# Optimization experiments

Hardware: AMD Instinct MI355X
Metric: run time of the kernel (lower is better)

## Reference

```python
import jax, jax.numpy as jnp
import numpy as np

EPS = 1e-5

def avg_pool3s2(x):
    # AvgPool2d(kernel=3, stride=2, no padding) on NCHW
    s = jax.lax.reduce_window(x, 0.0, jax.lax.add, (1, 1, 3, 3), (1, 1, 2, 2), 'VALID')
    return s / 9.0

def conv1x1(x, W):
    # x: [n,c,h,w], W: [out,c]
    return jnp.einsum('nchw,oc->nohw', x, W)

def batchnorm(x, g, b):
    # training-mode BN over (N,H,W), biased variance (matches torch normalization)
    m = x.mean(axis=(0, 2, 3), keepdims=True)
    v = x.var(axis=(0, 2, 3), keepdims=True)
    return (x - m) * jax.lax.rsqrt(v + EPS) * g[None, :, None, None] + b[None, :, None, None]

def coord_features(hp, wp):
    # [8, hp, wp]: xmin, ymin, xmax, ymax, xctr, yctr, 1/W, 1/H
    w = jnp.arange(wp, dtype=jnp.float32)
    h = jnp.arange(hp, dtype=jnp.float32)
    xmin = w / wp * 2 - 1
    xmax = (w + 1) / wp * 2 - 1
    xctr = (xmin + xmax) / 2
    ymin = h / hp * 2 - 1
    ymax = (h + 1) / hp * 2 - 1
    yctr = (ymin + ymax) / 2
    bx = lambda a: jnp.broadcast_to(a[None, :], (hp, wp))
    by = lambda a: jnp.broadcast_to(a[:, None], (hp, wp))
    const = lambda v: jnp.full((hp, wp), v, dtype=jnp.float32)
    return jnp.stack([bx(xmin), by(ymin), bx(xmax), by(ymax), bx(xctr), by(yctr),
                      const(1.0 / wp), const(1.0 / hp)], axis=0)

def resize_bilinear_ac(x, H, W):
    # bilinear upsample with align_corners=True, x: [n,c,h,w]
    h, w = x.shape[2], x.shape[3]
    ys = jnp.linspace(0.0, h - 1.0, H)
    xs = jnp.linspace(0.0, w - 1.0, W)
    y0 = jnp.floor(ys).astype(jnp.int32); y1 = jnp.minimum(y0 + 1, h - 1); wy = (ys - y0)[None, None, :, None]
    x0 = jnp.floor(xs).astype(jnp.int32); x1 = jnp.minimum(x0 + 1, w - 1); wx = (xs - x0)[None, None, None, :]
    rows = x[:, :, y0, :] * (1 - wy) + x[:, :, y1, :] * wy          # [n,c,H,w]
    return rows[:, :, :, x0] * (1 - wx) + rows[:, :, :, x1] * wx    # [n,c,H,W]

def setup_inputs() -> dict:
    key = jax.random.key(0)
    ks = jax.random.split(key, 8)
    n, in_dim, hid, h, w = 4, 256, 10, 129, 129
    d = hid + 8  # 18
    return {
        'p_fea': jax.random.normal(ks[0], (n, in_dim, h, w), dtype=jnp.float32),
        'hu': jax.random.normal(ks[1], (n, hid, h, w), dtype=jnp.float32),
        'Wq': jax.random.normal(ks[2], (d, d), dtype=jnp.float32) * 0.05,
        'Wk': jax.random.normal(ks[3], (d, in_dim + 8), dtype=jnp.float32) * 0.05,
        'Wv': jax.random.normal(ks[4], (128, in_dim), dtype=jnp.float32) * 0.05,
        'g_v': jnp.ones((128,), dtype=jnp.float32),
        'b_v': jnp.zeros((128,), dtype=jnp.float32),
        'Wp': jax.random.normal(ks[5], (hid, 128), dtype=jnp.float32) * 0.05,
        'g_p': jnp.ones((hid,), dtype=jnp.float32),
        'b_p': jnp.zeros((hid,), dtype=jnp.float32),
    }

def reference(p_fea, hu, Wq, Wk, Wv, g_v, b_v, Wp, g_p, b_p):
    n, c, h, w = p_fea.shape
    p = avg_pool3s2(p_fea)   # [n,256,hp,wp]
    u = avg_pool3s2(hu)      # [n,10,hp,wp]
    hp, wp = p.shape[2], p.shape[3]
    L = hp * wp
    coord = jnp.broadcast_to(coord_features(hp, wp)[None], (n, 8, hp, wp))
    query = conv1x1(jnp.concatenate([u, coord], axis=1), Wq).reshape(n, -1, L).transpose(0, 2, 1)  # [n,L,18]
    key_t = conv1x1(jnp.concatenate([p, coord], axis=1), Wk).reshape(n, -1, L)                      # [n,18,L]
    val = jax.nn.relu(batchnorm(conv1x1(p, Wv), g_v, b_v)).reshape(n, 128, L)                       # [n,128,L]
    energy = jnp.einsum('nlc,ncm->nlm', query, key_t)            # [n,L,L]
    attn = jax.nn.softmax(energy, axis=-1)
    ctx = jnp.einsum('ncm,nlm->ncl', val, attn).reshape(n, 128, hp, wp)
    ctx = jax.nn.relu(batchnorm(conv1x1(ctx, Wp), g_p, b_p))     # [n,10,hp,wp]
    return resize_bilinear_ac(ctx, h, w)                          # [n,10,h,w]
```

## Files before the change

kernel.cpp:

```cpp
#include <hip/hip_runtime.h>
#include <hip/hip_bf16.h>
#include <cstdint>

#define NN   4
#define LL   4096
#define DD   18
#define CVV  128
#define CIN  256
#define CUU  10
#define HH   129
#define COO  10

typedef unsigned short ushort_t;
typedef __attribute__((ext_vector_type(8))) short short8v;
typedef __attribute__((ext_vector_type(4))) short short4v;
typedef __attribute__((ext_vector_type(4))) float f32x4;

#define PB_OFF   ((size_t)0)
#define OP_OFF   ((size_t)2097152)
#define VAL_OFF  ((size_t)2260992)
#define QT_OFF   ((size_t)3309568)
#define KT_OFF   ((size_t)3571712)
#define VT_OFF   ((size_t)3833856)
#define VSC_OFF  ((size_t)4882432)
#define VSH_OFF  ((size_t)4882560)
#define S2_OFF   ((size_t)4882688)
#define SH2_OFF  ((size_t)4882704)
#define PART_OFF ((size_t)4882720)
#define PART2_OFF ((size_t)4915488)
#define KMAX_OFF ((size_t)4916768)

static __device__ __forceinline__ ushort_t f2bf(float x) {
    unsigned int u = __float_as_uint(x);
    unsigned int r = (u + 0x7fffu + ((u >> 16) & 1u)) >> 16;
    return (ushort_t)r;
}
static __device__ __forceinline__ float bf2f(ushort_t b) {
    return __uint_as_float(((unsigned int)b) << 16);
}
static __device__ __forceinline__ unsigned int pk2(float a, float b) {
    return (unsigned int)f2bf(a) | ((unsigned int)f2bf(b) << 16);
}

static __device__ __forceinline__ void gload16(const void* g, void* l) {
    __builtin_amdgcn_global_load_lds(
        (const __attribute__((address_space(1))) void*)g,
        (__attribute__((address_space(3))) void*)l, 16, 0, 0);
}

__global__ __launch_bounds__(256) void pool_bf_kernel(const float* __restrict__ src,
                                                      ushort_t* __restrict__ dst,
                                                      int* __restrict__ kz) {
    if (kz != nullptr && blockIdx.x == 0 && threadIdx.x < 128) kz[threadIdx.x] = 0;
    int b = blockIdx.x;
    int plane = b >> 4;
    int rg = b & 15;
    __shared__ float rows[9][132];
    const float* sp = src + (size_t)plane * (HH * HH) + (size_t)(rg * 8) * HH;
    #pragma unroll
    for (int j = 0; j < 9; ++j) {
        if (threadIdx.x < HH) rows[j][threadIdx.x] = sp[(size_t)j * HH + threadIdx.x];
    }
    __syncthreads();
    int row = threadIdx.x >> 6, ow = threadIdx.x & 63;
    const float* r0 = rows[2 * row];
    const float* r1 = rows[2 * row + 1];
    const float* r2 = rows[2 * row + 2];
    int x = 2 * ow;
    float sum = r0[x] + r0[x + 1] + r0[x + 2]
              + r1[x] + r1[x + 1] + r1[x + 2]
              + r2[x] + r2[x + 1] + r2[x + 2];
    dst[(size_t)plane * 4096 + (size_t)(rg * 4 + row) * 64 + ow] = f2bf(sum * (1.0f / 9.0f));
}

__global__ __launch_bounds__(256, 2) void qkval_kernel(const ushort_t* __restrict__ pb,
                                                       const float* __restrict__ hu,
                                                       const float* __restrict__ Wq,
                                                       const float* __restrict__ Wk,
                                                       const float* __restrict__ Wv,
                                                       ushort_t* __restrict__ qt,
                                                       char* __restrict__ kt_c,
                                                       int* __restrict__ kmaxb,
                                                       ushort_t* __restrict__ val,
                                                       float* __restrict__ part) {
    __shared__ __align__(16) char smem[36864];
    int tid = threadIdx.x;

    if (blockIdx.x < 256) {
        float (*kacc)[64][21] = (float(*)[64][21])smem;
        int n = blockIdx.x >> 6;
        int mb = blockIdx.x & 63;
        int mloc = tid & 63;
        int cs = tid >> 6;
        int m = mb * 64 + mloc;
        int hi = m >> 6, wi = m & 63;

        float coord[8];
        coord[0] = wi * (2.0f / 64.0f) - 1.0f;
        coord[1] = hi * (2.0f / 64.0f) - 1.0f;
        coord[2] = (wi + 1) * (2.0f / 64.0f) - 1.0f;
        coord[3] = (hi + 1) * (2.0f / 64.0f) - 1.0f;
        coord[4] = 0.5f * (coord[0] + coord[2]);
        coord[5] = 0.5f * (coord[1] + coord[3]);
        coord[6] = 1.0f / 64.0f;
        coord[7] = 1.0f / 64.0f;

        {
            float acc[DD];
            #pragma unroll
            for (int o = 0; o < DD; ++o) acc[o] = 0.0f;
            const ushort_t* pc = pb + ((size_t)(n * CIN + cs * 64)) * LL + m;
            for (int c0 = 0; c0 < 64; ++c0) {
                float pv = bf2f(pc[(size_t)c0 * LL]);
                const float* wr = Wk + (cs * 64 + c0);
                #pragma unroll
                for (int o = 0; o < DD; ++o) acc[o] = fmaf(pv, wr[o * 264], acc[o]);
            }
            if (cs == 3) {
                #pragma unroll
                for (int j = 0; j < 8; ++j) {
                    float cv = coord[j];
                    #pragma unroll
                    for (int o = 0; o < DD; ++o) acc[o] = fmaf(cv, Wk[o * 264 + CIN + j], acc[o]);
                }
            }
            #pragma unroll
            for (int o = 0; o < DD; ++o) kacc[cs][mloc][o] = acc[o];
        }
        if (cs == 0) {
            float acc[DD];
            #pragma unroll
            for (int o = 0; o < DD; ++o) acc[o] = 0.0f;
            const float* hub = hu + ((size_t)(n * CUU)) * (HH * HH) + (size_t)(2 * hi) * HH + 2 * wi;
            for (int cq = 0; cq < CUU; ++cq) {
                const float* s = hub + (size_t)cq * (HH * HH);
                float uv = (s[0] + s[1] + s[2]
                          + s[HH] + s[HH + 1] + s[HH + 2]
                          + s[2 * HH] + s[2 * HH + 1] + s[2 * HH + 2]) * (1.0f / 9.0f);
                #pragma unroll
                for (int o = 0; o < DD; ++o) acc[o] = fmaf(uv, Wq[o * DD + cq], acc[o]);
            }
            #pragma unroll
            for (int j = 0; j < 8; ++j) {
                float cv = coord[j];
                #pragma unroll
                for (int o = 0; o < DD; ++o) acc[o] = fmaf(cv, Wq[o * DD + CUU + j], acc[o]);
            }
            union { short8v v[4]; ushort_t s[32]; } pk;
            #pragma unroll
            for (int o = 0; o < 32; ++o) pk.s[o] = (o < DD) ? f2bf(acc[o]) : (ushort_t)0;
            short8v* qrow = (short8v*)(qt + ((size_t)(n * LL) + m) * 32);
            #pragma unroll
            for (int j = 0; j < 4; ++j) qrow[j] = pk.v[j];
        }
        __syncthreads();
        {
            int j = cs;
            union { short8v v; ushort_t s[8]; } pk;
            #pragma unroll
            for (int i = 0; i < 8; ++i) {
                int o = j * 8 + i;
                float v = 0.0f;
                if (o < DD)
                    v = kacc[0][mloc][o] + kacc[1][mloc][o] + kacc[2][mloc][o] + kacc[3][mloc][o];
                pk.s[i] = (o < DD) ? f2bf(v) : (ushort_t)0;
            }
            int byte = ((mloc << 6) | (j << 4)) ^ (((mloc >> 1) & 7) << 4);
            *(short8v*)(kt_c + (size_t)n * 262144 + (size_t)mb * 4096 + byte) = pk.v;

            int mb8[8];
            #pragma unroll
            for (int i = 0; i < 8; ++i) mb8[i] = (int)(pk.s[i] & 0x7fffu);
            #pragma unroll
            for (int off = 1; off < 64; off <<= 1) {
                #pragma unroll
                for (int i = 0; i < 8; ++i) {
                    int ov = __shfl_xor(mb8[i], off);
                    mb8[i] = max(mb8[i], ov);
                }
            }
            if (mloc == 0) {
                #pragma unroll
                for (int i = 0; i < 8; ++i)
                    atomicMax(&kmaxb[n * 32 + cs * 8 + i], mb8[i] << 16);
            }
        }
    } else {
        float (*Wt)[36] = (float(*)[36])smem;
        int b = blockIdx.x - 256;
        int n  = b >> 7;
        int cb = (b >> 5) & 3;
        int mb = b & 31;
        int cg = tid >> 5;
        int mg = tid & 31;
        int ch0 = cb * 32;
        int m0 = mb * 128;

        {
            int c4 = tid & 63;
            int chq = tid >> 6;
            #pragma unroll
            for (int j = 0; j < 8; ++j) {
                int ch = chq * 8 + j;
                float4 v = *(const float4*)&Wv[(size_t)(ch0 + ch) * CIN + c4 * 4];
                Wt[c4 * 4 + 0][ch] = v.x;
                Wt[c4 * 4 + 1][ch] = v.y;
                Wt[c4 * 4 + 2][ch] = v.z;
                Wt[c4 * 4 + 3][ch] = v.w;
            }
        }
        __syncthreads();

        const ushort_t* pbb = pb + (size_t)n * CIN * LL + m0 + mg * 4;
        f32x4 a0 = {0.f,0.f,0.f,0.f}, a1 = {0.f,0.f,0.f,0.f};
        f32x4 a2 = {0.f,0.f,0.f,0.f}, a3 = {0.f,0.f,0.f,0.f};

        #pragma unroll 4
        for (int c = 0; c < CIN; ++c) {
            short4v ps = *(const short4v*)(pbb + (size_t)c * LL);
            f32x4 pv;
            pv[0] = bf2f((ushort_t)ps[0]); pv[1] = bf2f((ushort_t)ps[1]);
            pv[2] = bf2f((ushort_t)ps[2]); pv[3] = bf2f((ushort_t)ps[3]);
            f32x4 wv = *(const f32x4*)&Wt[c][cg * 4];
            a0 += pv * wv.x;
            a1 += pv * wv.y;
            a2 += pv * wv.z;
            a3 += pv * wv.w;
        }

        size_t out = ((size_t)(n * CVV + ch0 + cg * 4)) * LL + m0 + mg * 4;
        union { short4v v; ushort_t s[4]; } w0, w1, w2, w3;
        #pragma unroll
        for (int i = 0; i < 4; ++i) {
            w0.s[i] = f2bf(a0[i]); w1.s[i] = f2bf(a1[i]);
            w2.s[i] = f2bf(a2[i]); w3.s[i] = f2bf(a3[i]);
        }
        *(short4v*)&val[out]          = w0.v;
        *(short4v*)&val[out + LL]     = w1.v;
        *(short4v*)&val[out + 2*LL]   = w2.v;
        *(short4v*)&val[out + 3*LL]   = w3.v;

        float s1[4], s2[4];
        s1[0] = a0[0]+a0[1]+a0[2]+a0[3]; s2[0] = a0[0]*a0[0]+a0[1]*a0[1]+a0[2]*a0[2]+a0[3]*a0[3];
        s1[1] = a1[0]+a1[1]+a1[2]+a1[3]; s2[1] = a1[0]*a1[0]+a1[1]*a1[1]+a1[2]*a1[2]+a1[3]*a1[3];
        s1[2] = a2[0]+a2[1]+a2[2]+a2[3]; s2[2] = a2[0]*a2[0]+a2[1]*a2[1]+a2[2]*a2[2]+a2[3]*a2[3];
        s1[3] = a3[0]+a3[1]+a3[2]+a3[3]; s2[3] = a3[0]*a3[0]+a3[1]*a3[1]+a3[2]*a3[2]+a3[3]*a3[3];
        #pragma unroll
        for (int off = 1; off < 32; off <<= 1) {
            #pragma unroll
            for (int i = 0; i < 4; ++i) {
                s1[i] += __shfl_xor(s1[i], off);
                s2[i] += __shfl_xor(s2[i], off);
            }
        }
        if (mg == 0) {
            #pragma unroll
            for (int i = 0; i < 4; ++i) {
                part[(((size_t)b * 8 + cg) * 4 + i) * 2]     = s1[i];
                part[(((size_t)b * 8 + cg) * 4 + i) * 2 + 1] = s2[i];
            }
        }
    }
}

__global__ __launch_bounds__(128) void bn_finalize_v_kernel(const float* __restrict__ part,
                                                            const float* __restrict__ g,
                                                            const float* __restrict__ bta,
                                                            float* __restrict__ scale,
                                                            float* __restrict__ shift) {
    int ch = threadIdx.x;
    if (ch >= CVV) return;
    int cb = ch >> 5;
    int cg = (ch & 31) >> 2;
    int i = ch & 3;
    float s1 = 0.0f, s2 = 0.0f;
    for (int n = 0; n < NN; ++n) {
        for (int mb = 0; mb < 32; ++mb) {
            int b = n * 128 + cb * 32 + mb;
            size_t idx = (((size_t)b * 8 + cg) * 4 + i) * 2;
            s1 += part[idx];
            s2 += part[idx + 1];
        }
    }
    float mean = s1 * (1.0f / (NN * LL));
    float var = s2 * (1.0f / (NN * LL)) - mean * mean;
    float inv = rsqrtf(var + 1e-5f);
    float sc = g[ch] * inv;
    scale[ch] = sc;
    shift[ch] = bta[ch] - mean * sc;
}

__global__ __launch_bounds__(256) void bn_apply2_kernel(const ushort_t* __restrict__ val,
                                                        const float* __restrict__ scale,
                                                        const float* __restrict__ shift,
                                                        char* __restrict__ vt_c) {
    int t = blockIdx.x * 256 + threadIdx.x;
    int mq = t & 511;
    int ch = (t >> 9) & 127;
    int n = t >> 16;
    int m0 = mq * 8;
    short8v vs = *(const short8v*)(val + ((size_t)(n * CVV + ch)) * LL + m0);
    float sc = scale[ch], sh = shift[ch];
    union { short8v v; ushort_t s[8]; } pk;
    #pragma unroll
    for (int i = 0; i < 8; ++i)
        pk.s[i] = f2bf(fmaxf(fmaf(bf2f((ushort_t)vs[i]), sc, sh), 0.0f));
    int tile = m0 >> 5, mloc = m0 & 31;
    size_t byte = (size_t)n * 1048576 + (size_t)tile * 8192
                + (size_t)(((ch << 6) | (mloc << 1)) ^ ((ch & 7) << 4));
    *(short8v*)(vt_c + byte) = pk.v;
}

__global__ __launch_bounds__(256, 4) void attn_swz_kernel(const ushort_t* __restrict__ qt,
                                                          const char* __restrict__ kt_c,
                                                          const char* __restrict__ vt_c,
                                                          const int* __restrict__ kmaxb,
                                                          const float* __restrict__ Wp,
                                                          float* __restrict__ ypart,
                                                          float* __restrict__ Lp) {
    int orig = blockIdx.x;
    int xcd = orig & 7;
    int idx = orig >> 3;
    int qb = idx >> 1;
    int combo = xcd * 2 + (idx & 1);
    int n = combo >> 2;
    int sM = combo & 3;
    int T0 = sM * 32;

    int tid = threadIdx.x;
    int w = tid >> 6, lane = tid & 63, c = lane & 15, g = lane >> 4;
    int l0w = qb * 64 + w * 16;

    __shared__ __align__(16) ushort_t K_t[2][1024];
    __shared__ __align__(16) ushort_t V_t[2][4096];
    __shared__ __align__(16) uint4 exch[4][64];
    __shared__ float Wpl[COO][CVV];

    for (int i = tid; i < COO * CVV; i += 256) Wpl[i >> 7][i & 127] = Wp[i];

    const char* ktb = kt_c + (size_t)n * 262144;
    const char* vtb = vt_c + (size_t)n * 1048576;

    short8v qf = *(const short8v*)(qt + (((size_t)n * LL + l0w + c) << 5) + g * 8);
    int vxor = (c & 7) << 4;

    float Mq = 0.0f;
    {
        const int* km = kmaxb + n * 32 + g * 8;
        #pragma unroll
        for (int i = 0; i < 8; ++i) {
            float kv = __int_as_float(km[i]);
            float aq = __uint_as_float(((unsigned int)((ushort_t)qf[i]) & 0x7fffu) << 16);
            Mq = fmaf(aq, kv, Mq);
        }
        Mq += __shfl_xor(Mq, 16);
        Mq += __shfl_xor(Mq, 32);
    }

    f32x4 O[8];
    #pragma unroll
    for (int i = 0; i < 8; ++i) O[i] = (f32x4){0.f, 0.f, 0.f, 0.f};
    float Lacc = 0.0f;

    int kby0, kby1;
    {
        int kr0 = c, kr1 = 16 + c;
        kby0 = ((kr0 << 6) | (g << 4)) ^ (((kr0 >> 1) & 7) << 4);
        kby1 = ((kr1 << 6) | (g << 4)) ^ (((kr1 >> 1) & 7) << 4);
    }
    int srcA = ((g & 1) << 5) + c;
    int toff = (g >> 1) * 8;

    {
        int T = T0;
        const char* ks = ktb + (size_t)(T >> 1) * 4096 + (T & 1) * 2048 + w * 1024 + lane * 16;
        if (w < 2) gload16(ks, (char*)K_t[0] + w * 1024);
        const char* vs = vtb + (size_t)T * 8192 + w * 2048 + lane * 16;
        gload16(vs, (char*)V_t[0] + w * 2048);
        gload16(vs + 1024, (char*)V_t[0] + w * 2048 + 1024);
    }
    __syncthreads();
    int buf = 0;
    for (int mt = 0; mt < 32; ++mt) {
        if (mt + 1 < 32) {
            int T = T0 + mt + 1;
            const char* ks = ktb + (size_t)(T >> 1) * 4096 + (T & 1) * 2048 + w * 1024 + lane * 16;
            if (w < 2) gload16(ks, (char*)K_t[buf ^ 1] + w * 1024);
            const char* vs = vtb + (size_t)T * 8192 + w * 2048 + lane * 16;
            gload16(vs, (char*)V_t[buf ^ 1] + w * 2048);
            gload16(vs + 1024, (char*)V_t[buf ^ 1] + w * 2048 + 1024);
        }
        const char* kb = (const char*)K_t[buf];
        short8v kf0 = *(const short8v*)(kb + kby0);
        short8v kf1 = *(const short8v*)(kb + kby1);
        f32x4 S0 = __builtin_amdgcn_mfma_f32_16x16x32_bf16(kf0, qf, (f32x4){0.f,0.f,0.f,0.f}, 0, 0, 0);
        f32x4 S1 = __builtin_amdgcn_mfma_f32_16x16x32_bf16(kf1, qf, (f32x4){0.f,0.f,0.f,0.f}, 0, 0, 0);
        float p0[4], p1[4];
        #pragma unroll
        for (int r = 0; r < 4; ++r) {
            p0[r] = __expf(S0[r] - Mq);
            p1[r] = __expf(S1[r] - Mq);
            Lacc += p0[r] + p1[r];
        }
        exch[w][lane] = (uint4){ pk2(p0[0], p0[1]), pk2(p0[2], p0[3]),
                                 pk2(p1[0], p1[1]), pk2(p1[2], p1[3]) };
        const char* eb = (const char*)&exch[w][0];
        uint2 ua = *(const uint2*)(eb + srcA * 16 + toff);
        uint2 ub = *(const uint2*)(eb + (srcA + 16) * 16 + toff);
        union { unsigned int u[4]; short8v v; } pa;
        pa.u[0] = ua.x; pa.u[1] = ua.y; pa.u[2] = ub.x; pa.u[3] = ub.y;
        const char* vb = (const char*)V_t[buf];
        __builtin_amdgcn_s_setprio(1);
        #pragma unroll
        for (int ct = 0; ct < 8; ++ct) {
            int vby = (((ct * 16 + c) << 6) | (g << 4)) ^ vxor;
            short8v vf = *(const short8v*)(vb + vby);
            O[ct] = __builtin_amdgcn_mfma_f32_16x16x32_bf16(pa.v, vf, O[ct], 0, 0, 0);
        }
        __builtin_amdgcn_s_setprio(0);
        __syncthreads();
        buf ^= 1;
    }
    Lacc += __shfl_xor(Lacc, 16);
    Lacc += __shfl_xor(Lacc, 32);
    if (g == 0)
        Lp[sM * (NN * LL) + n * LL + l0w + c] = Lacc;

    float yp[COO][4];
    #pragma unroll
    for (int o = 0; o < COO; ++o)
        #pragma unroll
        for (int r = 0; r < 4; ++r) yp[o][r] = 0.0f;
    #pragma unroll
    for (int ct = 0; ct < 8; ++ct) {
        #pragma unroll
        for (int o = 0; o < COO; ++o) {
            float wv = Wpl[o][ct * 16 + c];
            #pragma unroll
            for (int r = 0; r < 4; ++r)
                yp[o][r] = fmaf(O[ct][r], wv, yp[o][r]);
        }
    }
    #pragma unroll
    for (int off = 1; off < 16; off <<= 1) {
        #pragma unroll
        for (int o = 0; o < COO; ++o)
            #pragma unroll
            for (int r = 0; r < 4; ++r)
                yp[o][r] += __shfl_xor(yp[o][r], off);
    }
    if (c == 0) {
        #pragma unroll
        for (int r = 0; r < 4; ++r) {
            size_t yrow = (size_t)(sM * (NN * LL) + n * LL + l0w + g * 4 + r);
            #pragma unroll
            for (int o = 0; o < COO; ++o)
                ypart[yrow * COO + o] = yp[o][r];
        }
    }
}

__global__ __launch_bounds__(256) void combine4b_kernel(const float* __restrict__ ypart,
                                                        const float* __restrict__ Lp,
                                                        float* __restrict__ out_pre,
                                                        float* __restrict__ part2) {
    int idx = blockIdx.x * 256 + threadIdx.x;
    int n = idx >> 12;
    int l = idx & 4095;
    int nl = n * LL + l;
    float inv = 1.0f / (Lp[nl] + Lp[16384 + nl] + Lp[2 * 16384 + nl] + Lp[3 * 16384 + nl]);
    const float* y0 = ypart + (size_t)nl * COO;
    const float* y1 = ypart + ((size_t)16384 + nl) * COO;
    const float* y2 = ypart + ((size_t)(2 * 16384) + nl) * COO;
    const float* y3 = ypart + ((size_t)(3 * 16384) + nl) * COO;
    float ov[COO];
    #pragma unroll
    for (int o = 0; o < COO; ++o) {
        ov[o] = (y0[o] + y1[o] + y2[o] + y3[o]) * inv;
        out_pre[((size_t)(n * COO + o)) * LL + l] = ov[o];
    }
    float p1[COO], p2[COO];
    #pragma unroll
    for (int o = 0; o < COO; ++o) { p1[o] = ov[o]; p2[o] = ov[o] * ov[o]; }
    #pragma unroll
    for (int off = 1; off < 64; off <<= 1) {
        #pragma unroll
        for (int o = 0; o < COO; ++o) {
            p1[o] += __shfl_xor(p1[o], off);
            p2[o] += __shfl_xor(p2[o], off);
        }
    }
    __shared__ float rs1[4][COO], rs2[4][COO];
    int w = threadIdx.x >> 6, lane = threadIdx.x & 63;
    if (lane == 0) {
        #pragma unroll
        for (int o = 0; o < COO; ++o) { rs1[w][o] = p1[o]; rs2[w][o] = p2[o]; }
    }
    __syncthreads();
    if (threadIdx.x < COO) {
        int o = threadIdx.x;
        float a = rs1[0][o] + rs1[1][o] + rs1[2][o] + rs1[3][o];
        float b = rs2[0][o] + rs2[1][o] + rs2[2][o] + rs2[3][o];
        part2[((size_t)blockIdx.x * COO + o) * 2]     = a;
        part2[((size_t)blockIdx.x * COO + o) * 2 + 1] = b;
    }
}

__global__ __launch_bounds__(64) void bn_finalize2_kernel(const float* __restrict__ part2,
                                                          const float* __restrict__ g,
                                                          const float* __restrict__ bta,
                                                          float* __restrict__ scale,
                                                          float* __restrict__ shift) {
    int ch = threadIdx.x;
    if (ch >= COO) return;
    float s1 = 0.0f, s2 = 0.0f;
    for (int b = 0; b < 64; ++b) {
        s1 += part2[((size_t)b * COO + ch) * 2];
        s2 += part2[((size_t)b * COO + ch) * 2 + 1];
    }
    float mean = s1 * (1.0f / (NN * LL));
    float var = s2 * (1.0f / (NN * LL)) - mean * mean;
    float inv = rsqrtf(var + 1e-5f);
    float sc = g[ch] * inv;
    scale[ch] = sc;
    shift[ch] = bta[ch] - mean * sc;
}

__global__ __launch_bounds__(256) void resize_kernel(const float* __restrict__ out_pre,
                                                     const float* __restrict__ scale,
                                                     const float* __restrict__ shift,
                                                     float* __restrict__ out,
                                                     int total) {
    int idx = blockIdx.x * 256 + threadIdx.x;
    if (idx >= total) return;
    int ow = idx % HH;
    int t = idx / HH;
    int oh = t % HH;
    int t2 = t / HH;
    int o = t2 % COO;
    int n = t2 / COO;

    const float r = 63.0f / 128.0f;
    float y = oh * r;
    float x = ow * r;
    int y0 = (int)y;
    int x0 = (int)x;
    float wy = y - y0;
    float wx = x - x0;
    int y1 = min(y0 + 1, 63);
    int x1 = min(x0 + 1, 63);

    const float* base = out_pre + ((size_t)(n * COO + o)) * LL;
    float sc = scale[o], sh = shift[o];
    float v00 = fmaxf(fmaf(base[y0 * 64 + x0], sc, sh), 0.0f);
    float v01 = fmaxf(fmaf(base[y0 * 64 + x1], sc, sh), 0.0f);
    float v10 = fmaxf(fmaf(base[y1 * 64 + x0], sc, sh), 0.0f);
    float v11 = fmaxf(fmaf(base[y1 * 64 + x1], sc, sh), 0.0f);
    float top = v00 * (1.0f - wx) + v01 * wx;
    float bot = v10 * (1.0f - wx) + v11 * wx;
    out[idx] = top * (1.0f - wy) + bot * wy;
}

extern "C" void kernel_launch(void* const* d_in, const int* in_sizes, int n_in,
                              void* d_out, int out_size, void* d_ws, size_t ws_size,
                              hipStream_t stream) {
    (void)in_sizes; (void)n_in; (void)out_size; (void)ws_size;
    const float* p_fea = (const float*)d_in[0];
    const float* hu    = (const float*)d_in[1];
    const float* Wq    = (const float*)d_in[2];
    const float* Wk    = (const float*)d_in[3];
    const float* Wv    = (const float*)d_in[4];
    const float* g_v   = (const float*)d_in[5];
    const float* b_v   = (const float*)d_in[6];
    const float* Wp    = (const float*)d_in[7];
    const float* g_p   = (const float*)d_in[8];
    const float* b_p   = (const float*)d_in[9];

    float* ws = (float*)d_ws;
    ushort_t* pbb     = (ushort_t*)(ws + PB_OFF);
    float*    out_pre = ws + OP_OFF;
    ushort_t* valb    = (ushort_t*)(ws + VAL_OFF);
    ushort_t* qtb     = (ushort_t*)(ws + QT_OFF);
    char*     ktb     = (char*)(ws + KT_OFF);
    char*     vtb     = (char*)(ws + VT_OFF);
    float*    Lpart   = ws + VAL_OFF;
    float*    ypart   = ws + VAL_OFF + 65536;
    float*    vscale  = ws + VSC_OFF;
    float*    vshift  = ws + VSH_OFF;
    float*    scale2  = ws + S2_OFF;
    float*    shift2  = ws + SH2_OFF;
    float*    part    = ws + PART_OFF;
    float*    part2   = ws + PART2_OFF;
    int*      kmaxb   = (int*)(ws + KMAX_OFF);

    pool_bf_kernel<<<NN * CIN * 16, 256, 0, stream>>>(p_fea, pbb, kmaxb);
    qkval_kernel<<<768, 256, 0, stream>>>(pbb, hu, Wq, Wk, Wv, qtb, ktb, kmaxb, valb, part);
    bn_finalize_v_kernel<<<1, 128, 0, stream>>>(part, g_v, b_v, vscale, vshift);
    bn_apply2_kernel<<<(NN * CVV * 512) / 256, 256, 0, stream>>>(valb, vscale, vshift, vtb);
    attn_swz_kernel<<<1024, 256, 0, stream>>>(qtb, ktb, vtb, kmaxb, Wp, ypart, Lpart);
    combine4b_kernel<<<(NN * LL) / 256, 256, 0, stream>>>(ypart, Lpart, out_pre, part2);
    bn_finalize2_kernel<<<1, 64, 0, stream>>>(part2, g_p, b_p, scale2, shift2);
    {
        int total = NN * COO * HH * HH;
        resize_kernel<<<(total + 255) / 256, 256, 0, stream>>>(out_pre, scale2, shift2,
                                                               (float*)d_out, total);
    }
}
```

Measured before the change: 140.5 us.

## Pool into channel-interleaved layout and compute value conv with bf16 MFMA

The pooling kernel now handles 8 channels per block and writes the pooled features in a channel-interleaved [n, c/8, L, 8] bf16 layout with 16-byte stores. The value 1x1 conv drops its scalar FMA loop in favor of 16x16x32 bf16 MFMA instructions that read this layout directly, and the K projection reads 8 channels per vector load. BN partial sums are reorganized per block and channel, and the finalize kernel is updated to match. Weights are rounded to bf16 on the fly, which adds some rounding error, and the value output is now written as scattered 2-byte stores.

```diff
diff --git a/kernel.cpp b/kernel.cpp
--- a/kernel.cpp
+++ b/kernel.cpp
@@ -13,10 +13,9 @@
 
 typedef unsigned short ushort_t;
 typedef __attribute__((ext_vector_type(8))) short short8v;
-typedef __attribute__((ext_vector_type(4))) short short4v;
 typedef __attribute__((ext_vector_type(4))) float f32x4;
 
-#define PB_OFF   ((size_t)0)
+#define PT_OFF   ((size_t)0)
 #define OP_OFF   ((size_t)2097152)
 #define VAL_OFF  ((size_t)2260992)
 #define QT_OFF   ((size_t)3309568)
@@ -27,8 +26,8 @@
 #define S2_OFF   ((size_t)4882688)
 #define SH2_OFF  ((size_t)4882704)
 #define PART_OFF ((size_t)4882720)
-#define PART2_OFF ((size_t)4915488)
-#define KMAX_OFF ((size_t)4916768)
+#define PART2_OFF ((size_t)4948256)
+#define KMAX_OFF ((size_t)4949536)
 
 static __device__ __forceinline__ ushort_t f2bf(float x) {
     unsigned int u = __float_as_uint(x);
@@ -48,42 +47,54 @@
         (__attribute__((address_space(3))) void*)l, 16, 0, 0);
 }
 
-__global__ __launch_bounds__(256) void pool_bf_kernel(const float* __restrict__ src,
-                                                      ushort_t* __restrict__ dst,
+__global__ __launch_bounds__(256) void pool_pt_kernel(const float* __restrict__ src,
+                                                      ushort_t* __restrict__ pt,
                                                       int* __restrict__ kz) {
     if (kz != nullptr && blockIdx.x == 0 && threadIdx.x < 128) kz[threadIdx.x] = 0;
     int b = blockIdx.x;
-    int plane = b >> 4;
     int rg = b & 15;
-    __shared__ float rows[9][132];
-    const float* sp = src + (size_t)plane * (HH * HH) + (size_t)(rg * 8) * HH;
-    #pragma unroll
-    for (int j = 0; j < 9; ++j) {
-        if (threadIdx.x < HH) rows[j][threadIdx.x] = sp[(size_t)j * HH + threadIdx.x];
+    int cg = (b >> 4) & 31;
+    int n  = b >> 9;
+
+    __shared__ float rows[8][9][132];
+    const float* base = src + ((size_t)(n * CIN + cg * 8)) * (HH * HH) + (size_t)(rg * 8) * HH;
+    for (int t = threadIdx.x; t < 8 * 9 * 132; t += 256) {
+        int col = t % 132;
+        int rr  = (t / 132) % 9;
+        int ch  = t / (132 * 9);
+        if (col < HH)
+            rows[ch][rr][col] = base[(size_t)ch * (HH * HH) + (size_t)rr * HH + col];
     }
     __syncthreads();
+
     int row = threadIdx.x >> 6, ow = threadIdx.x & 63;
-    const float* r0 = rows[2 * row];
-    const float* r1 = rows[2 * row + 1];
-    const float* r2 = rows[2 * row + 2];
     int x = 2 * ow;
-    float sum = r0[x] + r0[x + 1] + r0[x + 2]
-              + r1[x] + r1[x + 1] + r1[x + 2]
-              + r2[x] + r2[x + 1] + r2[x + 2];
-    dst[(size_t)plane * 4096 + (size_t)(rg * 4 + row) * 64 + ow] = f2bf(sum * (1.0f / 9.0f));
-}
-
-__global__ __launch_bounds__(256, 2) void qkval_kernel(const ushort_t* __restrict__ pb,
-                                                       const float* __restrict__ hu,
-                                                       const float* __restrict__ Wq,
-                                                       const float* __restrict__ Wk,
-                                                       const float* __restrict__ Wv,
-                                                       ushort_t* __restrict__ qt,
-                                                       char* __restrict__ kt_c,
-                                                       int* __restrict__ kmaxb,
-                                                       ushort_t* __restrict__ val,
-                                                       float* __restrict__ part) {
-    __shared__ __align__(16) char smem[36864];
+    union { short8v v; ushort_t s[8]; } pk;
+    #pragma unroll
+    for (int ch = 0; ch < 8; ++ch) {
+        const float* r0 = rows[ch][2 * row];
+        const float* r1 = rows[ch][2 * row + 1];
+        const float* r2 = rows[ch][2 * row + 2];
+        float sum = r0[x] + r0[x + 1] + r0[x + 2]
+                  + r1[x] + r1[x + 1] + r1[x + 2]
+                  + r2[x] + r2[x + 1] + r2[x + 2];
+        pk.s[ch] = f2bf(sum * (1.0f / 9.0f));
+    }
+    int m = (rg * 4 + row) * 64 + ow;
+    *(short8v*)(pt + (((size_t)(n * 32 + cg)) * 4096 + m) * 8) = pk.v;
+}
+
+__global__ __launch_bounds__(256, 2) void qkval2_kernel(const ushort_t* __restrict__ pt,
+                                                        const float* __restrict__ hu,
+                                                        const float* __restrict__ Wq,
+                                                        const float* __restrict__ Wk,
+                                                        const float* __restrict__ Wv,
+                                                        ushort_t* __restrict__ qt,
+                                                        char* __restrict__ kt_c,
+                                                        int* __restrict__ kmaxb,
+                                                        ushort_t* __restrict__ val,
+                                                        float* __restrict__ part) {
+    __shared__ __align__(16) char smem[21504];
     int tid = threadIdx.x;
 
     if (blockIdx.x < 256) {
@@ -109,12 +120,17 @@
             float acc[DD];
             #pragma unroll
             for (int o = 0; o < DD; ++o) acc[o] = 0.0f;
-            const ushort_t* pc = pb + ((size_t)(n * CIN + cs * 64)) * LL + m;
-            for (int c0 = 0; c0 < 64; ++c0) {
-                float pv = bf2f(pc[(size_t)c0 * LL]);
-                const float* wr = Wk + (cs * 64 + c0);
-                #pragma unroll
-                for (int o = 0; o < DD; ++o) acc[o] = fmaf(pv, wr[o * 264], acc[o]);
+            #pragma unroll 2
+            for (int j = 0; j < 8; ++j) {
+                union { short8v v; ushort_t s[8]; } ps;
+                ps.v = *(const short8v*)(pt + (((size_t)(n * 32 + cs * 8 + j)) * 4096 + m) * 8);
+                #pragma unroll
+                for (int i = 0; i < 8; ++i) {
+                    float pv = bf2f(ps.s[i]);
+                    const float* wr = Wk + (cs * 64 + j * 8 + i);
+                    #pragma unroll
+                    for (int o = 0; o < DD; ++o) acc[o] = fmaf(pv, wr[o * 264], acc[o]);
+                }
             }
             if (cs == 3) {
                 #pragma unroll
@@ -186,101 +202,87 @@
             }
         }
     } else {
-        float (*Wt)[36] = (float(*)[36])smem;
-        int b = blockIdx.x - 256;
-        int n  = b >> 7;
-        int cb = (b >> 5) & 3;
-        int mb = b & 31;
-        int cg = tid >> 5;
-        int mg = tid & 31;
-        int ch0 = cb * 32;
-        int m0 = mb * 128;
-
-        {
-            int c4 = tid & 63;
-            int chq = tid >> 6;
-            #pragma unroll
-            for (int j = 0; j < 8; ++j) {
-                int ch = chq * 8 + j;
-                float4 v = *(const float4*)&Wv[(size_t)(ch0 + ch) * CIN + c4 * 4];
-                Wt[c4 * 4 + 0][ch] = v.x;
-                Wt[c4 * 4 + 1][ch] = v.y;
-                Wt[c4 * 4 + 2][ch] = v.z;
-                Wt[c4 * 4 + 3][ch] = v.w;
-            }
-        }
-        __syncthreads();
-
-        const ushort_t* pbb = pb + (size_t)n * CIN * LL + m0 + mg * 4;
-        f32x4 a0 = {0.f,0.f,0.f,0.f}, a1 = {0.f,0.f,0.f,0.f};
-        f32x4 a2 = {0.f,0.f,0.f,0.f}, a3 = {0.f,0.f,0.f,0.f};
-
-        #pragma unroll 4
-        for (int c = 0; c < CIN; ++c) {
-            short4v ps = *(const short4v*)(pbb + (size_t)c * LL);
-            f32x4 pv;
-            pv[0] = bf2f((ushort_t)ps[0]); pv[1] = bf2f((ushort_t)ps[1]);
-            pv[2] = bf2f((ushort_t)ps[2]); pv[3] = bf2f((ushort_t)ps[3]);
-            f32x4 wv = *(const f32x4*)&Wt[c][cg * 4];
-            a0 += pv * wv.x;
-            a1 += pv * wv.y;
-            a2 += pv * wv.z;
-            a3 += pv * wv.w;
-        }
-
-        size_t out = ((size_t)(n * CVV + ch0 + cg * 4)) * LL + m0 + mg * 4;
-        union { short4v v; ushort_t s[4]; } w0, w1, w2, w3;
-        #pragma unroll
-        for (int i = 0; i < 4; ++i) {
-            w0.s[i] = f2bf(a0[i]); w1.s[i] = f2bf(a1[i]);
-            w2.s[i] = f2bf(a2[i]); w3.s[i] = f2bf(a3[i]);
-        }
-        *(short4v*)&val[out]          = w0.v;
-        *(short4v*)&val[out + LL]     = w1.v;
-        *(short4v*)&val[out + 2*LL]   = w2.v;
-        *(short4v*)&val[out + 3*LL]   = w3.v;
-
-        float s1[4], s2[4];
-        s1[0] = a0[0]+a0[1]+a0[2]+a0[3]; s2[0] = a0[0]*a0[0]+a0[1]*a0[1]+a0[2]*a0[2]+a0[3]*a0[3];
-        s1[1] = a1[0]+a1[1]+a1[2]+a1[3]; s2[1] = a1[0]*a1[0]+a1[1]*a1[1]+a1[2]*a1[2]+a1[3]*a1[3];
-        s1[2] = a2[0]+a2[1]+a2[2]+a2[3]; s2[2] = a2[0]*a2[0]+a2[1]*a2[1]+a2[2]*a2[2]+a2[3]*a2[3];
-        s1[3] = a3[0]+a3[1]+a3[2]+a3[3]; s2[3] = a3[0]*a3[0]+a3[1]*a3[1]+a3[2]*a3[2]+a3[3]*a3[3];
-        #pragma unroll
-        for (int off = 1; off < 32; off <<= 1) {
-            #pragma unroll
-            for (int i = 0; i < 4; ++i) {
-                s1[i] += __shfl_xor(s1[i], off);
-                s2[i] += __shfl_xor(s2[i], off);
-            }
-        }
-        if (mg == 0) {
-            #pragma unroll
-            for (int i = 0; i < 4; ++i) {
-                part[(((size_t)b * 8 + cg) * 4 + i) * 2]     = s1[i];
-                part[(((size_t)b * 8 + cg) * 4 + i) * 2 + 1] = s2[i];
-            }
-        }
-    }
-}
-
-__global__ __launch_bounds__(128) void bn_finalize_v_kernel(const float* __restrict__ part,
-                                                            const float* __restrict__ g,
-                                                            const float* __restrict__ bta,
-                                                            float* __restrict__ scale,
-                                                            float* __restrict__ shift) {
+        int b2 = blockIdx.x - 256;
+        int n  = b2 >> 6;
+        int mb = b2 & 63;
+        int m0 = mb * 64;
+        int w = tid >> 6, lane = tid & 63, cl = lane & 15, g = lane >> 4;
+
+        f32x4 acc[2][4];
+        #pragma unroll
+        for (int t = 0; t < 2; ++t)
+            #pragma unroll
+            for (int mt = 0; mt < 4; ++mt) acc[t][mt] = (f32x4){0.f, 0.f, 0.f, 0.f};
+
+        #pragma unroll 2
+        for (int kc = 0; kc < 8; ++kc) {
+            short8v bfr[4];
+            const ushort_t* pb2 = pt + (((size_t)(n * 32 + kc * 4 + g)) * 4096) * 8;
+            #pragma unroll
+            for (int mt = 0; mt < 4; ++mt)
+                bfr[mt] = *(const short8v*)(pb2 + (size_t)(m0 + mt * 16 + cl) * 8);
+            #pragma unroll
+            for (int t = 0; t < 2; ++t) {
+                int ch = (2 * w + t) * 16 + cl;
+                const float* wr = Wv + (size_t)ch * CIN + kc * 32 + 8 * g;
+                float4 wa = *(const float4*)wr;
+                float4 wb = *(const float4*)(wr + 4);
+                union { short8v v; ushort_t s[8]; } af;
+                af.s[0] = f2bf(wa.x); af.s[1] = f2bf(wa.y); af.s[2] = f2bf(wa.z); af.s[3] = f2bf(wa.w);
+                af.s[4] = f2bf(wb.x); af.s[5] = f2bf(wb.y); af.s[6] = f2bf(wb.z); af.s[7] = f2bf(wb.w);
+                #pragma unroll
+                for (int mt = 0; mt < 4; ++mt)
+                    acc[t][mt] = __builtin_amdgcn_mfma_f32_16x16x32_bf16(af.v, bfr[mt], acc[t][mt], 0, 0, 0);
+            }
+        }
+
+        #pragma unroll
+        for (int t = 0; t < 2; ++t) {
+            float s1[4] = {0.f, 0.f, 0.f, 0.f}, s2[4] = {0.f, 0.f, 0.f, 0.f};
+            #pragma unroll
+            for (int mt = 0; mt < 4; ++mt) {
+                #pragma unroll
+                for (int r = 0; r < 4; ++r) {
+                    float v = acc[t][mt][r];
+                    s1[r] += v;
+                    s2[r] = fmaf(v, v, s2[r]);
+                    int ch = (2 * w + t) * 16 + g * 4 + r;
+                    val[((size_t)(n * CVV + ch)) * LL + m0 + mt * 16 + cl] = f2bf(v);
+                }
+            }
+            #pragma unroll
+            for (int off = 1; off < 16; off <<= 1) {
+                #pragma unroll
+                for (int r = 0; r < 4; ++r) {
+                    s1[r] += __shfl_xor(s1[r], off);
+                    s2[r] += __shfl_xor(s2[r], off);
+                }
+            }
+            if (cl == 0) {
+                #pragma unroll
+                for (int r = 0; r < 4; ++r) {
+                    int ch = (2 * w + t) * 16 + g * 4 + r;
+                    size_t idx = (((size_t)b2) * CVV + ch) * 2;
+                    part[idx]     = s1[r];
+                    part[idx + 1] = s2[r];
+                }
+            }
+        }
+    }
+}
+
+__global__ __launch_bounds__(128) void bn_finalize_v2_kernel(const float* __restrict__ part,
+                                                             const float* __restrict__ g,
+                                                             const float* __restrict__ bta,
+                                                             float* __restrict__ scale,
+                                                             float* __restrict__ shift) {
     int ch = threadIdx.x;
     if (ch >= CVV) return;
-    int cb = ch >> 5;
-    int cg = (ch & 31) >> 2;
-    int i = ch & 3;
     float s1 = 0.0f, s2 = 0.0f;
-    for (int n = 0; n < NN; ++n) {
-        for (int mb = 0; mb < 32; ++mb) {
-            int b = n * 128 + cb * 32 + mb;
-            size_t idx = (((size_t)b * 8 + cg) * 4 + i) * 2;
-            s1 += part[idx];
-            s2 += part[idx + 1];
-        }
+    for (int b = 0; b < 256; ++b) {
+        size_t idx = ((size_t)b * CVV + ch) * 2;
+        s1 += part[idx];
+        s2 += part[idx + 1];
     }
     float mean = s1 * (1.0f / (NN * LL));
     float var = s2 * (1.0f / (NN * LL)) - mean * mean;
@@ -577,7 +579,7 @@
     const float* b_p   = (const float*)d_in[9];
 
     float* ws = (float*)d_ws;
-    ushort_t* pbb     = (ushort_t*)(ws + PB_OFF);
+    ushort_t* ptb     = (ushort_t*)(ws + PT_OFF);
     float*    out_pre = ws + OP_OFF;
     ushort_t* valb    = (ushort_t*)(ws + VAL_OFF);
     ushort_t* qtb     = (ushort_t*)(ws + QT_OFF);
@@ -593,9 +595,9 @@
     float*    part2   = ws + PART2_OFF;
     int*      kmaxb   = (int*)(ws + KMAX_OFF);
 
-    pool_bf_kernel<<<NN * CIN * 16, 256, 0, stream>>>(p_fea, pbb, kmaxb);
-    qkval_kernel<<<768, 256, 0, stream>>>(pbb, hu, Wq, Wk, Wv, qtb, ktb, kmaxb, valb, part);
-    bn_finalize_v_kernel<<<1, 128, 0, stream>>>(part, g_v, b_v, vscale, vshift);
+    pool_pt_kernel<<<NN * 32 * 16, 256, 0, stream>>>(p_fea, ptb, kmaxb);
+    qkval2_kernel<<<512, 256, 0, stream>>>(ptb, hu, Wq, Wk, Wv, qtb, ktb, kmaxb, valb, part);
+    bn_finalize_v2_kernel<<<1, 128, 0, stream>>>(part, g_v, b_v, vscale, vshift);
     bn_apply2_kernel<<<(NN * CVV * 512) / 256, 256, 0, stream>>>(valb, vscale, vshift, vtb);
     attn_swz_kernel<<<1024, 256, 0, stream>>>(qtb, ktb, vtb, kmaxb, Wp, ypart, Lpart);
     combine4b_kernel<<<(NN * LL) / 256, 256, 0, stream>>>(ypart, Lpart, out_pre, part2);
```

Result: slower. 151.7 us (+7.9%).
